# Kernel optimization log

Measured on AMD Instinct MI355X. Metric: run time of the kernel, lower is better.

Reference implementation:

```python
import jax, jax.numpy as jnp
import numpy as np

N_NODES = 2_000_000
IN_CH = 64
OUT_CH = 128
NUM_GRAPHS = 16384


def setup_inputs() -> dict:
    key = jax.random.key(0)
    k1, k2, k3, k4 = jax.random.split(key, 4)
    x = jax.random.normal(k1, (N_NODES, IN_CH), dtype=jnp.float32)
    segment_ids = jnp.sort(
        jax.random.randint(k2, (N_NODES,), 0, NUM_GRAPHS, dtype=jnp.int64)
    )
    # nn.Linear(in, out): weight [out, in], bias [out]
    bound = 1.0 / np.sqrt(IN_CH)
    weight = jax.random.uniform(k3, (OUT_CH, IN_CH), dtype=jnp.float32,
                                minval=-bound, maxval=bound)
    bias = jax.random.uniform(k4, (OUT_CH,), dtype=jnp.float32,
                              minval=-bound, maxval=bound)
    return {"x": x, "segment_ids": segment_ids, "weight": weight,
            "bias": bias, "num_graphs": NUM_GRAPHS}


def reference(x, segment_ids, weight, bias, num_graphs):
    # Per-graph mean pooling (segment mean), then linear embed.
    sums = jax.ops.segment_sum(x, segment_ids, num_segments=num_graphs)  # [G, d]
    counts = jax.ops.segment_sum(jnp.ones((x.shape[0],), x.dtype),
                                 segment_ids, num_segments=num_graphs)  # [G]
    means = sums / counts[:, None]                                       # [G, d]
    return means @ weight.T + bias                                        # [G, out]
```

## Files before the change

### kernel.cpp

```cpp
#include <hip/hip_runtime.h>
#include <hip/hip_bf16.h>


#define IN_CH 64
#define OUT_CH 128
#define GPW 2
#define PBLK 256
#define LBLK 512
#define LGRID 512

typedef float f32x4 __attribute__((ext_vector_type(4)));

__device__ __forceinline__ void stream_seg(const float* __restrict__ x,
                                           int s0, int s1, int rs, int cq,
                                           float& sx, float& sy,
                                           float& sz, float& sw) {
    float4 a0 = make_float4(0.f, 0.f, 0.f, 0.f);
    float4 a1 = make_float4(0.f, 0.f, 0.f, 0.f);
    int r = s0;
    for (; r + 8 <= s1; r += 8) {
        const f32x4 v0 = __builtin_nontemporal_load(
            reinterpret_cast<const f32x4*>(x + (size_t)(r + rs) * IN_CH + cq));
        const f32x4 v1 = __builtin_nontemporal_load(
            reinterpret_cast<const f32x4*>(x + (size_t)(r + 4 + rs) * IN_CH + cq));
        a0.x += v0.x; a0.y += v0.y; a0.z += v0.z; a0.w += v0.w;
        a1.x += v1.x; a1.y += v1.y; a1.z += v1.z; a1.w += v1.w;
    }
    if (r + 4 <= s1) {
        const f32x4 v = __builtin_nontemporal_load(
            reinterpret_cast<const f32x4*>(x + (size_t)(r + rs) * IN_CH + cq));
        a0.x += v.x; a0.y += v.y; a0.z += v.z; a0.w += v.w;
        r += 4;
    }
    if (r + rs < s1) {
        const f32x4 v = __builtin_nontemporal_load(
            reinterpret_cast<const f32x4*>(x + (size_t)(r + rs) * IN_CH + cq));
        a1.x += v.x; a1.y += v.y; a1.z += v.z; a1.w += v.w;
    }
    sx = a0.x + a1.x; sy = a0.y + a1.y;
    sz = a0.z + a1.z; sw = a0.w + a1.w;
    sx += __shfl_xor(sx, 16); sy += __shfl_xor(sy, 16);
    sz += __shfl_xor(sz, 16); sw += __shfl_xor(sw, 16);
    sx += __shfl_xor(sx, 32); sy += __shfl_xor(sy, 32);
    sz += __shfl_xor(sz, 32); sw += __shfl_xor(sw, 32);
}

__global__ __launch_bounds__(PBLK, 8) void pool_kernel(
        const float* __restrict__ x, const int* __restrict__ ids,
        float* __restrict__ means, int N, int G) {
    const int t  = threadIdx.x;
    const int w  = blockIdx.x * (PBLK / 64) + (t >> 6);
    const int l  = t & 63;
    const int g0 = w * GPW;
    if (g0 >= G) return;

    const int tgt = g0 + ((l < 2) ? l : 2);
    int lo = 0, hi = N;
    {
        const int guess = (int)(((long long)tgt * (long long)N) / (long long)G);
        int wlo = guess - 4096; if (wlo < 0) wlo = 0;
        int whi = guess + 4096; if (whi > N) whi = N;
        const bool ok_lo = (wlo == 0) || (ids[wlo - 1] < tgt);
        const bool ok_hi = (whi == N) || (ids[whi] >= tgt);
        if (ok_lo && ok_hi) { lo = wlo; hi = whi; }
        while (lo < hi) {
            const int mid = (lo + hi) >> 1;
            if (ids[mid] < tgt) lo = mid + 1; else hi = mid;
        }
    }
    const int s0 = __shfl(lo, 0);
    const int s1 = __shfl(lo, 1);
    const int s2 = __shfl(lo, 2);

    const int rs = l >> 4;
    const int cq = (l & 15) << 2;

    float sx, sy, sz, sw;

    stream_seg(x, s0, s1, rs, cq, sx, sy, sz, sw);
    {
        const float cnt = (float)(s1 - s0);
        if (l < 16) {
            f32x4 m; m.x = sx / cnt; m.y = sy / cnt; m.z = sz / cnt; m.w = sw / cnt;
            *reinterpret_cast<f32x4*>(means + (size_t)g0 * IN_CH + cq) = m;
        }
    }

    if (g0 + 1 < G) {
        stream_seg(x, s1, s2, rs, cq, sx, sy, sz, sw);
        const float cnt = (float)(s2 - s1);
        if (l < 16) {
            f32x4 m; m.x = sx / cnt; m.y = sy / cnt; m.z = sz / cnt; m.w = sw / cnt;
            *reinterpret_cast<f32x4*>(means + (size_t)(g0 + 1) * IN_CH + cq) = m;
        }
    }
}

__global__ __launch_bounds__(LBLK) void linear_kernel(
        const float* __restrict__ means, const float* __restrict__ W,
        const float* __restrict__ bias, float* __restrict__ out, int G) {
    __shared__ float w_lds[IN_CH * 129];
    const int t = threadIdx.x;
    for (int i = t; i < OUT_CH * IN_CH; i += LBLK) {
        const int o = i >> 6, c = i & 63;
        w_lds[c * 129 + o] = W[i];
    }
    __syncthreads();

    const int wv = t >> 6, l = t & 63;
    const int cq = (l & 15) << 2;
    const float b0 = bias[l], b1 = bias[l + 64];

    for (int g = blockIdx.x * (LBLK / 64) + wv; g < G; g += LGRID * (LBLK / 64)) {
        const f32x4 s = *reinterpret_cast<const f32x4*>(
            means + (size_t)g * IN_CH + cq);
        const float m0 = s.x, m1 = s.y, m2 = s.z, m3 = s.w;

        float o0 = b0, o1 = b1;
        #pragma unroll
        for (int c = 0; c < IN_CH; ++c) {
            float m;
            switch (c & 3) {
                case 0:  m = __shfl(m0, c >> 2); break;
                case 1:  m = __shfl(m1, c >> 2); break;
                case 2:  m = __shfl(m2, c >> 2); break;
                default: m = __shfl(m3, c >> 2); break;
            }
            o0 = fmaf(w_lds[c * 129 + l],      m, o0);
            o1 = fmaf(w_lds[c * 129 + l + 64], m, o1);
        }
        out[(size_t)g * OUT_CH + l]      = o0;
        out[(size_t)g * OUT_CH + l + 64] = o1;
    }
}

#define WPB 8
#define BLOCK (WPB * 64)
__global__ __launch_bounds__(BLOCK) void fused_pool_linear_kernel(
        const float* __restrict__ x, const int* __restrict__ ids,
        const float* __restrict__ W, const float* __restrict__ bias,
        float* __restrict__ out, int N, int G) {
    __shared__ float w_lds[IN_CH * 129];
    const int t  = threadIdx.x;
    const int wv = t >> 6;
    const int l  = t & 63;
    const int g  = blockIdx.x * WPB + wv;

    int s0 = 0, s1 = 0;
    if (g < G) {
        const int target = g + (l & 1);
        int lo = 0, hi = N;
        const int guess = (int)(((long long)target * (long long)N) / (long long)G);
        int wlo = guess - 4096; if (wlo < 0) wlo = 0;
        int whi = guess + 4096; if (whi > N) whi = N;
        const bool ok_lo = (wlo == 0) || (ids[wlo - 1] < target);
        const bool ok_hi = (whi == N) || (ids[whi] >= target);
        if (ok_lo && ok_hi) { lo = wlo; hi = whi; }
        while (lo < hi) {
            const int mid = (lo + hi) >> 1;
            if (ids[mid] < target) lo = mid + 1; else hi = mid;
        }
        s0 = __shfl(lo, 0);
        s1 = __shfl(lo, 1);
    }
    for (int i = t; i < OUT_CH * IN_CH; i += BLOCK) {
        const int o = i >> 6, c = i & 63;
        w_lds[c * 129 + o] = W[i];
    }
    __syncthreads();
    if (g >= G) return;

    const int rs = l >> 4;
    const int cq = (l & 15) << 2;
    float sx, sy, sz, sw;
    stream_seg(x, s0, s1, rs, cq, sx, sy, sz, sw);
    const float cnt = (float)(s1 - s0);
    const float m0 = sx / cnt, m1 = sy / cnt, m2 = sz / cnt, m3 = sw / cnt;
    float o0 = bias[l], o1 = bias[l + 64];
    #pragma unroll
    for (int c = 0; c < IN_CH; ++c) {
        float m;
        switch (c & 3) {
            case 0:  m = __shfl(m0, c >> 2); break;
            case 1:  m = __shfl(m1, c >> 2); break;
            case 2:  m = __shfl(m2, c >> 2); break;
            default: m = __shfl(m3, c >> 2); break;
        }
        o0 = fmaf(w_lds[c * 129 + l],      m, o0);
        o1 = fmaf(w_lds[c * 129 + l + 64], m, o1);
    }
    out[(size_t)g * OUT_CH + l]      = o0;
    out[(size_t)g * OUT_CH + l + 64] = o1;
}

extern "C" void kernel_launch(void* const* d_in, const int* in_sizes, int n_in,
                              void* d_out, int out_size, void* d_ws, size_t ws_size,
                              hipStream_t stream) {
    const float* x    = (const float*)d_in[0];
    const int*   ids  = (const int*)d_in[1];
    const float* W    = (const float*)d_in[2];
    const float* bias = (const float*)d_in[3];
    float* out = (float*)d_out;

    const int N = in_sizes[1];
    const int G = out_size / OUT_CH;

    const size_t means_bytes = (size_t)G * IN_CH * sizeof(float);

    if (ws_size >= means_bytes) {
        float* means = (float*)d_ws;
        const int waves   = (G + GPW - 1) / GPW;
        const int pblocks = (waves + (PBLK / 64) - 1) / (PBLK / 64);
        pool_kernel<<<pblocks, PBLK, 0, stream>>>(x, ids, means, N, G);
        linear_kernel<<<LGRID, LBLK, 0, stream>>>(means, W, bias, out, G);
    } else {
        const int blocks = (G + WPB - 1) / WPB;
        fused_pool_linear_kernel<<<blocks, BLOCK, 0, stream>>>(
            x, ids, W, bias, out, N, G);
    }
}
```

Baseline: 119.0 us.

## Fuse pooling and linear into persistent work-stealing kernel with deeper unroll

Replaces the separate pool and linear kernels with one persistent kernel of FGRID blocks, in which each wave takes graphs from a global atomic counter and does the segment search, the streaming sum and the linear projection in place. This removes the intermediate means buffer round-trip and the second launch, and balances uneven segment sizes through dynamic stealing. The streaming loop is also unrolled to 16 rows with four accumulators for more memory parallelism. The cost is an added memset launch, one atomic per graph, and the weight-to-LDS load repeated in every persistent block.

Result: slower. 240.5 us (+102.2%).

```diff
diff --git a/kernel.cpp b/kernel.cpp
--- a/kernel.cpp
+++ b/kernel.cpp
@@ -4,117 +4,88 @@
 
 #define IN_CH 64
 #define OUT_CH 128
-#define GPW 2
-#define PBLK 256
-#define LBLK 512
-#define LGRID 512
+#define FBLK 512
+#define FGRID 1024
 
 typedef float f32x4 __attribute__((ext_vector_type(4)));
+
+__device__ __forceinline__ f32x4 ntload(const float* p) {
+    return __builtin_nontemporal_load(reinterpret_cast<const f32x4*>(p));
+}
 
 __device__ __forceinline__ void stream_seg(const float* __restrict__ x,
                                            int s0, int s1, int rs, int cq,
                                            float& sx, float& sy,
                                            float& sz, float& sw) {
-    float4 a0 = make_float4(0.f, 0.f, 0.f, 0.f);
-    float4 a1 = make_float4(0.f, 0.f, 0.f, 0.f);
+    f32x4 a0 = {0.f, 0.f, 0.f, 0.f};
+    f32x4 a1 = {0.f, 0.f, 0.f, 0.f};
+    f32x4 a2 = {0.f, 0.f, 0.f, 0.f};
+    f32x4 a3 = {0.f, 0.f, 0.f, 0.f};
     int r = s0;
-    for (; r + 8 <= s1; r += 8) {
-        const f32x4 v0 = __builtin_nontemporal_load(
-            reinterpret_cast<const f32x4*>(x + (size_t)(r + rs) * IN_CH + cq));
-        const f32x4 v1 = __builtin_nontemporal_load(
-            reinterpret_cast<const f32x4*>(x + (size_t)(r + 4 + rs) * IN_CH + cq));
-        a0.x += v0.x; a0.y += v0.y; a0.z += v0.z; a0.w += v0.w;
-        a1.x += v1.x; a1.y += v1.y; a1.z += v1.z; a1.w += v1.w;
+    for (; r + 16 <= s1; r += 16) {
+        const f32x4 v0 = ntload(x + (size_t)(r + rs)      * IN_CH + cq);
+        const f32x4 v1 = ntload(x + (size_t)(r + 4 + rs)  * IN_CH + cq);
+        const f32x4 v2 = ntload(x + (size_t)(r + 8 + rs)  * IN_CH + cq);
+        const f32x4 v3 = ntload(x + (size_t)(r + 12 + rs) * IN_CH + cq);
+        a0 += v0; a1 += v1; a2 += v2; a3 += v3;
     }
-    if (r + 4 <= s1) {
-        const f32x4 v = __builtin_nontemporal_load(
-            reinterpret_cast<const f32x4*>(x + (size_t)(r + rs) * IN_CH + cq));
-        a0.x += v.x; a0.y += v.y; a0.z += v.z; a0.w += v.w;
-        r += 4;
+    for (; r + 4 <= s1; r += 4) {
+        a0 += ntload(x + (size_t)(r + rs) * IN_CH + cq);
     }
     if (r + rs < s1) {
-        const f32x4 v = __builtin_nontemporal_load(
-            reinterpret_cast<const f32x4*>(x + (size_t)(r + rs) * IN_CH + cq));
-        a1.x += v.x; a1.y += v.y; a1.z += v.z; a1.w += v.w;
+        a1 += ntload(x + (size_t)(r + rs) * IN_CH + cq);
     }
-    sx = a0.x + a1.x; sy = a0.y + a1.y;
-    sz = a0.z + a1.z; sw = a0.w + a1.w;
+    const f32x4 a = (a0 + a1) + (a2 + a3);
+    sx = a.x; sy = a.y; sz = a.z; sw = a.w;
     sx += __shfl_xor(sx, 16); sy += __shfl_xor(sy, 16);
     sz += __shfl_xor(sz, 16); sw += __shfl_xor(sw, 16);
     sx += __shfl_xor(sx, 32); sy += __shfl_xor(sy, 32);
     sz += __shfl_xor(sz, 32); sw += __shfl_xor(sw, 32);
 }
 
-__global__ __launch_bounds__(PBLK, 8) void pool_kernel(
+__global__ __launch_bounds__(FBLK) void fused_steal_kernel(
         const float* __restrict__ x, const int* __restrict__ ids,
-        float* __restrict__ means, int N, int G) {
-    const int t  = threadIdx.x;
-    const int w  = blockIdx.x * (PBLK / 64) + (t >> 6);
-    const int l  = t & 63;
-    const int g0 = w * GPW;
-    if (g0 >= G) return;
-
-    const int tgt = g0 + ((l < 2) ? l : 2);
-    int lo = 0, hi = N;
-    {
-        const int guess = (int)(((long long)tgt * (long long)N) / (long long)G);
-        int wlo = guess - 4096; if (wlo < 0) wlo = 0;
-        int whi = guess + 4096; if (whi > N) whi = N;
-        const bool ok_lo = (wlo == 0) || (ids[wlo - 1] < tgt);
-        const bool ok_hi = (whi == N) || (ids[whi] >= tgt);
-        if (ok_lo && ok_hi) { lo = wlo; hi = whi; }
-        while (lo < hi) {
-            const int mid = (lo + hi) >> 1;
-            if (ids[mid] < tgt) lo = mid + 1; else hi = mid;
-        }
-    }
-    const int s0 = __shfl(lo, 0);
-    const int s1 = __shfl(lo, 1);
-    const int s2 = __shfl(lo, 2);
-
-    const int rs = l >> 4;
-    const int cq = (l & 15) << 2;
-
-    float sx, sy, sz, sw;
-
-    stream_seg(x, s0, s1, rs, cq, sx, sy, sz, sw);
-    {
-        const float cnt = (float)(s1 - s0);
-        if (l < 16) {
-            f32x4 m; m.x = sx / cnt; m.y = sy / cnt; m.z = sz / cnt; m.w = sw / cnt;
-            *reinterpret_cast<f32x4*>(means + (size_t)g0 * IN_CH + cq) = m;
-        }
-    }
-
-    if (g0 + 1 < G) {
-        stream_seg(x, s1, s2, rs, cq, sx, sy, sz, sw);
-        const float cnt = (float)(s2 - s1);
-        if (l < 16) {
-            f32x4 m; m.x = sx / cnt; m.y = sy / cnt; m.z = sz / cnt; m.w = sw / cnt;
-            *reinterpret_cast<f32x4*>(means + (size_t)(g0 + 1) * IN_CH + cq) = m;
-        }
-    }
-}
-
-__global__ __launch_bounds__(LBLK) void linear_kernel(
-        const float* __restrict__ means, const float* __restrict__ W,
-        const float* __restrict__ bias, float* __restrict__ out, int G) {
+        const float* __restrict__ W, const float* __restrict__ bias,
+        float* __restrict__ out, int* __restrict__ counter, int N, int G) {
     __shared__ float w_lds[IN_CH * 129];
     const int t = threadIdx.x;
-    for (int i = t; i < OUT_CH * IN_CH; i += LBLK) {
+    for (int i = t; i < OUT_CH * IN_CH; i += FBLK) {
         const int o = i >> 6, c = i & 63;
         w_lds[c * 129 + o] = W[i];
     }
     __syncthreads();
 
     const int wv = t >> 6, l = t & 63;
+    const int nwaves = FGRID * (FBLK / 64);
+    int g = blockIdx.x * (FBLK / 64) + wv;
+
+    const int rs = l >> 4;
     const int cq = (l & 15) << 2;
     const float b0 = bias[l], b1 = bias[l + 64];
 
-    for (int g = blockIdx.x * (LBLK / 64) + wv; g < G; g += LGRID * (LBLK / 64)) {
-        const f32x4 s = *reinterpret_cast<const f32x4*>(
-            means + (size_t)g * IN_CH + cq);
-        const float m0 = s.x, m1 = s.y, m2 = s.z, m3 = s.w;
+    while (g < G) {
+        const int tgt = g + (l & 1);
+        int lo = 0, hi = N;
+        {
+            const int guess = (int)(((long long)tgt * (long long)N) / (long long)G);
+            int wlo = guess - 4096; if (wlo < 0) wlo = 0;
+            int whi = guess + 4096; if (whi > N) whi = N;
+            const bool ok_lo = (wlo == 0) || (ids[wlo - 1] < tgt);
+            const bool ok_hi = (whi == N) || (ids[whi] >= tgt);
+            if (ok_lo && ok_hi) { lo = wlo; hi = whi; }
+            while (lo < hi) {
+                const int mid = (lo + hi) >> 1;
+                if (ids[mid] < tgt) lo = mid + 1; else hi = mid;
+            }
+        }
+        const int s0 = __shfl(lo, 0);
+        const int s1 = __shfl(lo, 1);
+
+        float sx, sy, sz, sw;
+        stream_seg(x, s0, s1, rs, cq, sx, sy, sz, sw);
+        const float cnt = (float)(s1 - s0);
+        const float m0 = sx / cnt, m1 = sy / cnt;
+        const float m2 = sz / cnt, m3 = sw / cnt;
 
         float o0 = b0, o1 = b1;
         #pragma unroll
@@ -131,6 +102,11 @@
         }
         out[(size_t)g * OUT_CH + l]      = o0;
         out[(size_t)g * OUT_CH + l + 64] = o1;
+
+        int tk = 0;
+        if (l == 0) tk = atomicAdd(counter, 1);
+        tk = __shfl(tk, 0);
+        g = nwaves + tk;
     }
 }
 
@@ -205,14 +181,11 @@
     const int N = in_sizes[1];
     const int G = out_size / OUT_CH;
 
-    const size_t means_bytes = (size_t)G * IN_CH * sizeof(float);
-
-    if (ws_size >= means_bytes) {
-        float* means = (float*)d_ws;
-        const int waves   = (G + GPW - 1) / GPW;
-        const int pblocks = (waves + (PBLK / 64) - 1) / (PBLK / 64);
-        pool_kernel<<<pblocks, PBLK, 0, stream>>>(x, ids, means, N, G);
-        linear_kernel<<<LGRID, LBLK, 0, stream>>>(means, W, bias, out, G);
+    if (ws_size >= sizeof(int)) {
+        int* counter = (int*)d_ws;
+        hipMemsetAsync(counter, 0, sizeof(int), stream);
+        fused_steal_kernel<<<FGRID, FBLK, 0, stream>>>(
+            x, ids, W, bias, out, counter, N, G);
     } else {
         const int blocks = (G + WPB - 1) / WPB;
         fused_pool_linear_kernel<<<blocks, BLOCK, 0, stream>>>(
```
